# Performance work log

Hardware: AMD Instinct MI355X
Metric: run time of the kernel (lower is better)

The kernel has to match this reference:

```python
import jax, jax.numpy as jnp
import numpy as np

B, C, N, T = 64, 16, 4096, 12   # batch, channels, num_nodes, timesteps
APT = 10                        # adaptive-embedding size
NUM_SUPPORTS = 3                # 2 fixed + 1 adaptive
ORDER = 2                       # diffusion hops


def _rand_adj(k):
    # random row-stochastic transition matrix (stand-in for normalized graph support)
    a = jax.random.uniform(k, (N, N), jnp.float32)
    return a / jnp.sum(a, axis=1, keepdims=True)


def setup_inputs() -> dict:
    key = jax.random.key(0)
    ks = jax.random.split(key, 7)
    x = jax.random.normal(ks[0], (B, C, N, T), jnp.float32)
    support0 = _rand_adj(ks[1])
    support1 = _rand_adj(ks[2])
    nodevec1 = jax.random.normal(ks[3], (N, APT), jnp.float32)
    nodevec2 = jax.random.normal(ks[4], (APT, N), jnp.float32)
    c_cat = C * (NUM_SUPPORTS * ORDER + 1)  # 7*C
    W = jax.random.normal(ks[5], (C, c_cat), jnp.float32) * 0.05  # 1x1 conv weight
    b = jnp.zeros((C,), jnp.float32)
    return dict(x=x, support0=support0, support1=support1,
                nodevec1=nodevec1, nodevec2=nodevec2, W=W, b=b)


def _nconv(x, a):
    # torch: einsum('ncvl,vw->ncwl')
    return jnp.einsum('bcnt,nm->bcmt', x, a)


def reference(x, support0, support1, nodevec1, nodevec2, W, b):
    # adaptive adjacency: softmax(relu(E1 @ E2), dim=1)
    adp = jax.nn.softmax(jax.nn.relu(nodevec1 @ nodevec2), axis=1)
    supports = [support0, support1, adp]
    outs = [x]
    for a in supports:  # small fixed loop over supports/hops
        x1 = _nconv(x, a)
        outs.append(x1)
        x2 = _nconv(x1, a)
        outs.append(x2)
    h = jnp.concatenate(outs, axis=1)            # [B, 7C, N, T]
    h = jnp.einsum('bknt,ck->bcnt', h, W) + b[None, :, None, None]  # 1x1 conv
    # dropout omitted (eval mode / deterministic reference)
    return x + h                                  # residual add
```

## Files before the change

kernel.cpp:

```cpp
#include <hip/hip_runtime.h>
#include <hip/hip_bf16.h>

#define B_  64
#define C_  16
#define N_  4096
#define T_  12
#define ROWS_ (B_ * T_ * C_)
#define NT_ 64

typedef __attribute__((ext_vector_type(4))) float f32x4;
typedef __attribute__((ext_vector_type(8))) short s16x8;
typedef __attribute__((ext_vector_type(4))) short s16x4;
typedef __attribute__((ext_vector_type(8))) int   i32x8;
typedef __attribute__((ext_vector_type(4))) int   i32x4;

__device__ __forceinline__ ushort f2bf(float f) {
    unsigned u = __builtin_bit_cast(unsigned, f);
    u += 0x7fffu + ((u >> 16) & 1u);
    return (ushort)(u >> 16);
}

__device__ __forceinline__ uchar f2fp8(float f) {
    float a = fabsf(f);
    unsigned s = (__builtin_bit_cast(unsigned, f) >> 24) & 0x80u;
    if (a >= 448.f) return (uchar)(s | 0x7E);
    if (a < 0.015625f) {
        int m = (int)rintf(a * 512.f);
        return (uchar)(s | (unsigned)m);
    }
    unsigned u = __builtin_bit_cast(unsigned, a);
    unsigned r = (u + 0x7FFFFu + ((u >> 20) & 1u)) >> 20;
    return (uchar)(s | (r - 960u));
}

__device__ __forceinline__ f32x4 mfma16x16x16bf16(s16x4 a, s16x4 b, f32x4 c) {
#if __has_builtin(__builtin_amdgcn_mfma_f32_16x16x16_bf16)
    return __builtin_amdgcn_mfma_f32_16x16x16_bf16(a, b, c, 0, 0, 0);
#elif __has_builtin(__builtin_amdgcn_mfma_f32_16x16x16bf16_1k)
    return __builtin_amdgcn_mfma_f32_16x16x16bf16_1k(a, b, c, 0, 0, 0);
#else
    f32x4 d = c;
    asm volatile("v_mfma_f32_16x16x16_bf16 %0, %1, %2, %0"
                 : "+v"(d) : "v"(a), "v"(b));
    return d;
#endif
}

typedef const __attribute__((address_space(1))) unsigned int* gas_t;
typedef __attribute__((address_space(3))) unsigned int* las_t;
__device__ __forceinline__ void gload16(const ushort* g, ushort* l) {
    __builtin_amdgcn_global_load_lds((gas_t)(const void*)g, (las_t)(void*)l, 16, 0, 0);
}
__device__ __forceinline__ void gload16b(const uchar* g, uchar* l) {
    __builtin_amdgcn_global_load_lds((gas_t)(const void*)g, (las_t)(void*)l, 16, 0, 0);
}

__global__ __launch_bounds__(256)
void pack_x(const float* __restrict__ x, ushort* __restrict__ X2,
            uchar* __restrict__ X8) {
    __shared__ float xs[16][32][13];
    const int t  = threadIdx.x;
    const int n0 = blockIdx.x * 32;
    const int b  = blockIdx.y;
    #pragma unroll
    for (int p0 = 0; p0 < 2; ++p0) {
        int p = p0 * 256 + t;
        int c = p >> 5, nn = p & 31;
        const float* src = x + (size_t)((b * 16 + c) * 4096 + n0 + nn) * 12;
        float tmp[12];
        *(float4*)(tmp)     = *(const float4*)(src);
        *(float4*)(tmp + 4) = *(const float4*)(src + 4);
        *(float4*)(tmp + 8) = *(const float4*)(src + 8);
        #pragma unroll
        for (int k = 0; k < 12; ++k) xs[c][nn][k] = tmp[k];
    }
    __syncthreads();
    #pragma unroll
    for (int i = 0; i < 24; ++i) {
        int e = i * 256 + t;
        int nn = e & 31, rowi = e >> 5;
        int tt = rowi >> 4, c = rowi & 15;
        float xv = xs[c][nn][tt];
        size_t row = (size_t)(b * 12 + tt) * 16 + c;
        X2[row * 4096 + n0 + nn] = f2bf(xv);
        X8[row * 4096 + n0 + nn] = f2fp8(xv);
    }
}

__global__ __launch_bounds__(256)
void transpose_fp8(const float* __restrict__ S, uchar* __restrict__ D, float scale) {
    __shared__ float ld[64][65];
    const int t  = threadIdx.x;
    const int m0 = blockIdx.x * 64;
    const int n0 = blockIdx.y * 64;
    #pragma unroll
    for (int it = 0; it < 4; ++it) {
        int row = it * 16 + (t >> 4);
        int col = (t & 15) * 4;
        float4 v = *(const float4*)&S[(size_t)(n0 + row) * 4096 + m0 + col];
        ld[row][col] = v.x; ld[row][col + 1] = v.y;
        ld[row][col + 2] = v.z; ld[row][col + 3] = v.w;
    }
    __syncthreads();
    #pragma unroll
    for (int it = 0; it < 8; ++it) {
        int mr = it * 8 + (t >> 5);
        int nc = (t & 31) * 2;
        ushort p = (ushort)f2fp8(ld[nc][mr] * scale) |
                   ((ushort)f2fp8(ld[nc + 1][mr] * scale) << 8);
        *(ushort*)&D[(size_t)(m0 + mr) * 4096 + n0 + nc] = p;
    }
}

__global__ __launch_bounds__(256)
void adp_rows(const float* __restrict__ e1, const float* __restrict__ e2,
              float* __restrict__ maxn, float* __restrict__ sumn) {
    const int n = blockIdx.x, t = threadIdx.x;
    __shared__ float se1[10];
    __shared__ float red[8];
    if (t < 10) se1[t] = e1[n * 10 + t];
    __syncthreads();
    float v[16];
    float mx = -1e30f;
    #pragma unroll
    for (int i = 0; i < 16; ++i) {
        int m = i * 256 + t;
        float s = 0.f;
        #pragma unroll
        for (int k = 0; k < 10; ++k) s += se1[k] * e2[k * 4096 + m];
        s = fmaxf(s, 0.f);
        v[i] = s;
        mx = fmaxf(mx, s);
    }
    for (int o = 32; o; o >>= 1) mx = fmaxf(mx, __shfl_down(mx, o));
    if ((t & 63) == 0) red[t >> 6] = mx;
    __syncthreads();
    if (t == 0) red[4] = fmaxf(fmaxf(red[0], red[1]), fmaxf(red[2], red[3]));
    __syncthreads();
    mx = red[4];
    float sm = 0.f;
    #pragma unroll
    for (int i = 0; i < 16; ++i) sm += __expf(v[i] - mx);
    for (int o = 32; o; o >>= 1) sm += __shfl_down(sm, o);
    __syncthreads();
    if ((t & 63) == 0) red[t >> 6] = sm;
    __syncthreads();
    if (t == 0) { maxn[n] = mx; sumn[n] = red[0] + red[1] + red[2] + red[3]; }
}

__global__ __launch_bounds__(256)
void adp_make(const float* __restrict__ e1, const float* __restrict__ e2,
              const float* __restrict__ maxn, const float* __restrict__ sumn,
              ushort* __restrict__ D) {
    __shared__ float se1[64][10];
    __shared__ float se2[10][64];
    const int t  = threadIdx.x;
    const int m0 = blockIdx.x * 64;
    const int n0 = blockIdx.y * 64;
    for (int i = t; i < 640; i += 256) ((float*)se1)[i] = e1[n0 * 10 + i];
    for (int i = t; i < 640; i += 256) {
        int k = i >> 6, m = i & 63;
        se2[k][m] = e2[k * 4096 + m0 + m];
    }
    __syncthreads();
    #pragma unroll
    for (int it = 0; it < 8; ++it) {
        int mr = it * 8 + (t >> 5);
        int nc = (t & 31) * 2;
        float v0 = 0.f, v1 = 0.f;
        #pragma unroll
        for (int k = 0; k < 10; ++k) {
            float e2v = se2[k][mr];
            v0 += se1[nc][k] * e2v;
            v1 += se1[nc + 1][k] * e2v;
        }
        v0 = fmaxf(v0, 0.f);
        v1 = fmaxf(v1, 0.f);
        float va = __expf(v0 - maxn[n0 + nc])     / sumn[n0 + nc];
        float vb = __expf(v1 - maxn[n0 + nc + 1]) / sumn[n0 + nc + 1];
        unsigned pack = (unsigned)f2bf(va) | ((unsigned)f2bf(vb) << 16);
        *(unsigned*)&D[(size_t)(m0 + mr) * 4096 + n0 + nc] = pack;
    }
}

__global__ __launch_bounds__(512, 2)
void gemm_mix(const ushort* __restrict__ Xp, const ushort* __restrict__ Bt,
              ushort* __restrict__ Yp, float* __restrict__ racc,
              const float* __restrict__ W, int cblk, int writeY, int initR) {
    __shared__ ushort lds[65536];
    const int tid  = threadIdx.x;
    const int lane = tid & 63;
    const int wid  = tid >> 6;
    const int wm   = wid >> 2;
    const int wn   = wid & 3;
    const int lr   = lane & 15;
    const int lq   = lane >> 4;
    const int fsw  = (lane & 7) << 3;

    int flat = blockIdx.y * gridDim.x + blockIdx.x;
    int swz  = (flat & 7) * 96 + (flat >> 3);
    const size_t r0 = (size_t)(swz >> 4) * 256;
    const size_t c0 = (size_t)(swz & 15) * 256;

#define AIDX(b, mi, ks) (((b) * 32768)          + (((((mi) * 32 + wm * 16 + lr) * 64) + (ks) * 32 + lq * 8) ^ fsw))
#define BIDX(b, nj, ks) (((b) * 32768 + 16384)  + ((((wn * 64 + (nj) * 16 + lr) * 64) + (ks) * 32 + lq * 8) ^ fsw))

#define STAGE(P, rg0, tt, h, mat)                                                      \
    {                                                                                  \
        ushort* _base = &lds[((tt) & 1) * 32768 + (mat) * 16384 + (h) * 8192];         \
        const size_t _k0 = (size_t)(tt) * 64;                                          \
        _Pragma("unroll")                                                              \
        for (int _i = 0; _i < 2; ++_i) {                                               \
            int _e   = (_i * 512 + tid) * 8;                                           \
            int _row = _e >> 6;                                                        \
            int _col = (_e & 63) ^ ((_row & 7) << 3);                                  \
            gload16(&(P)[((rg0) + (h) * 128 + _row) * 4096 + _k0 + _col], &_base[_e]); \
        }                                                                              \
    }

#define PHASE(MI0, STAGE_STMT)                                                                                 \
    {                                                                                                          \
        STAGE_STMT;                                                                                            \
        s16x8 a0 = *(const s16x8*)&lds[AIDX(b, (MI0),     0)];                                                 \
        s16x8 a1 = *(const s16x8*)&lds[AIDX(b, (MI0),     1)];                                                 \
        s16x8 a2 = *(const s16x8*)&lds[AIDX(b, (MI0) + 1, 0)];                                                 \
        s16x8 a3 = *(const s16x8*)&lds[AIDX(b, (MI0) + 1, 1)];                                                 \
        __builtin_amdgcn_s_barrier();                                                                          \
        __builtin_amdgcn_s_setprio(1);                                                                         \
        _Pragma("unroll")                                                                                      \
        for (int nj = 0; nj < 4; ++nj) {                                                                       \
            acc[(MI0)][nj]     = __builtin_amdgcn_mfma_f32_16x16x32_bf16(a0, bfr[nj][0], acc[(MI0)][nj], 0, 0, 0);     \
            acc[(MI0)][nj]     = __builtin_amdgcn_mfma_f32_16x16x32_bf16(a1, bfr[nj][1], acc[(MI0)][nj], 0, 0, 0);     \
            acc[(MI0) + 1][nj] = __builtin_amdgcn_mfma_f32_16x16x32_bf16(a2, bfr[nj][0], acc[(MI0) + 1][nj], 0, 0, 0); \
            acc[(MI0) + 1][nj] = __builtin_amdgcn_mfma_f32_16x16x32_bf16(a3, bfr[nj][1], acc[(MI0) + 1][nj], 0, 0, 0); \
        }                                                                                                      \
        __builtin_amdgcn_s_setprio(0);                                                                         \
    }

    f32x4 acc[8][4] = {};

    STAGE(Xp, r0, 0, 0, 0);
    STAGE(Xp, r0, 0, 1, 0);
    STAGE(Bt, c0, 0, 0, 1);
    STAGE(Bt, c0, 0, 1, 1);
    STAGE(Xp, r0, 1, 0, 0);
    STAGE(Bt, c0, 1, 0, 1);
    asm volatile("s_waitcnt vmcnt(4)" ::: "memory");
    __builtin_amdgcn_s_barrier();

    for (int t = 0; t < NT_; ++t) {
        const int b = t & 1;
        s16x8 bfr[4][2];
        if (t + 1 < NT_) STAGE(Xp, r0, t + 1, 1, 0);
        #pragma unroll
        for (int nj = 0; nj < 4; ++nj) {
            bfr[nj][0] = *(const s16x8*)&lds[BIDX(b, nj, 0)];
            bfr[nj][1] = *(const s16x8*)&lds[BIDX(b, nj, 1)];
        }
        PHASE(0, {});
        __builtin_amdgcn_s_barrier();
        PHASE(2, { if (t + 1 < NT_) STAGE(Bt, c0, t + 1, 1, 1); });
        __builtin_amdgcn_s_barrier();
        PHASE(4, { if (t + 2 < NT_) STAGE(Xp, r0, t + 2, 0, 0); });
        __builtin_amdgcn_s_barrier();
        PHASE(6, { if (t + 2 < NT_) STAGE(Bt, c0, t + 2, 0, 1); });
        if (t < NT_ - 2)       { asm volatile("s_waitcnt vmcnt(4)" ::: "memory"); }
        else if (t == NT_ - 2) { asm volatile("s_waitcnt vmcnt(0)" ::: "memory"); }
        __builtin_amdgcn_sched_barrier(0);
        __builtin_amdgcn_s_barrier();
    }

    if (writeY) {
        #pragma unroll
        for (int mi = 0; mi < 8; ++mi) {
            #pragma unroll
            for (int nj = 0; nj < 4; ++nj) {
                const int col = wn * 64 + nj * 16 + lr;
                #pragma unroll
                for (int r = 0; r < 4; ++r) {
                    const int rr = mi * 32 + wm * 16 + lq * 4 + r;
                    lds[(rr * 256 + col) ^ ((rr & 7) << 3)] = f2bf(acc[mi][nj][r]);
                }
            }
        }
        __syncthreads();
        #pragma unroll
        for (int it = 0; it < 16; ++it) {
            int e = it * 4096 + tid * 8;
            int row = e >> 8, colu = e & 255;
            s16x8 v = *(const s16x8*)&lds[e ^ ((row & 7) << 3)];
            *(s16x8*)&Yp[(r0 + row) * 4096 + c0 + colu] = v;
        }
    }

    {
        const float4 wv4 = *(const float4*)&W[(size_t)lr * 112 + cblk + lq * 4];
        s16x4 wf;
        wf[0] = (short)f2bf(wv4.x); wf[1] = (short)f2bf(wv4.y);
        wf[2] = (short)f2bf(wv4.z); wf[3] = (short)f2bf(wv4.w);
        #pragma unroll
        for (int mi = 0; mi < 8; ++mi) {
            #pragma unroll
            for (int nj = 0; nj < 4; ++nj) {
                s16x4 cb;
                cb[0] = (short)f2bf(acc[mi][nj][0]); cb[1] = (short)f2bf(acc[mi][nj][1]);
                cb[2] = (short)f2bf(acc[mi][nj][2]); cb[3] = (short)f2bf(acc[mi][nj][3]);
                f32x4 d = mfma16x16x16bf16(wf, cb, (f32x4){0.f, 0.f, 0.f, 0.f});
                const size_t row = r0 + (size_t)mi * 32 + wm * 16 + lq * 4;
                const size_t col = c0 + wn * 64 + nj * 16 + lr;
                if (initR) {
                    #pragma unroll
                    for (int r = 0; r < 4; ++r) racc[(row + r) * 4096 + col] = d[r];
                } else {
                    #pragma unroll
                    for (int r = 0; r < 4; ++r) {
                        float* p = &racc[(row + r) * 4096 + col];
                        *p += d[r];
                    }
                }
            }
        }
    }
#undef AIDX
#undef BIDX
#undef STAGE
#undef PHASE
}

__device__ __forceinline__ i32x8 ldfrag8(const uchar* lds8, int rbase, int row, int lq) {
    const int sw = (row & 7) << 4;
    const int b  = rbase + row * 128;
    i32x4 lo = *(const i32x4*)&lds8[b + ((lq * 32) ^ sw)];
    i32x4 hi = *(const i32x4*)&lds8[b + ((lq * 32 + 16) ^ sw)];
    return (i32x8){lo[0], lo[1], lo[2], lo[3], hi[0], hi[1], hi[2], hi[3]};
}

__global__ __launch_bounds__(512, 2)
void gemm_fp8(const uchar* __restrict__ Xp, const uchar* __restrict__ Bt,
              uchar* __restrict__ Yp, float* __restrict__ racc,
              const float* __restrict__ W, int cblk, int writeY, int initR,
              int sA, int sB, float ysc) {
    __shared__ uchar lds8[131072];
    const int tid  = threadIdx.x;
    const int lane = tid & 63;
    const int wid  = tid >> 6;
    const int wm   = wid >> 2;
    const int wn   = wid & 3;
    const int lr   = lane & 15;
    const int lq   = lane >> 4;

    int flat = blockIdx.y * gridDim.x + blockIdx.x;
    int swz  = (flat & 7) * 96 + (flat >> 3);
    const size_t r0 = (size_t)(swz >> 4) * 256;
    const size_t c0 = (size_t)(swz & 15) * 256;

#define STAGE8(P, rg0, tt, h, mat)                                                       \
    {                                                                                    \
        uchar* _base = &lds8[((tt) & 1) * 65536 + (mat) * 32768 + (h) * 16384];          \
        const size_t _k0 = (size_t)(tt) * 128;                                           \
        _Pragma("unroll")                                                                \
        for (int _i = 0; _i < 2; ++_i) {                                                 \
            int _e   = (_i * 512 + tid) * 16;                                            \
            int _row = _e >> 7;                                                          \
            int _col = (_e & 127) ^ ((_row & 7) << 4);                                   \
            gload16b(&(P)[((rg0) + (h) * 128 + _row) * 4096 + _k0 + _col], &_base[_e]);  \
        }                                                                                \
    }

    f32x4 acc[8][4] = {};

    STAGE8(Xp, r0, 0, 0, 0);
    STAGE8(Xp, r0, 0, 1, 0);
    STAGE8(Bt, c0, 0, 0, 1);
    STAGE8(Bt, c0, 0, 1, 1);
    STAGE8(Xp, r0, 1, 0, 0);
    STAGE8(Bt, c0, 1, 0, 1);
    asm volatile("s_waitcnt vmcnt(4)" ::: "memory");
    __builtin_amdgcn_s_barrier();

    for (int t = 0; t < 32; ++t) {
        const int bb = (t & 1) * 65536;
        i32x8 bf[4];
        if (t + 1 < 32) STAGE8(Xp, r0, t + 1, 1, 0);
        #pragma unroll
        for (int nj = 0; nj < 4; ++nj)
            bf[nj] = ldfrag8(lds8, bb + 32768, wn * 64 + nj * 16 + lr, lq);
        i32x8 af0 = ldfrag8(lds8, bb,       wm * 16 + lr, lq);
        i32x8 af1 = ldfrag8(lds8, bb,  32 + wm * 16 + lr, lq);
        i32x8 af2 = ldfrag8(lds8, bb,  64 + wm * 16 + lr, lq);
        i32x8 af3 = ldfrag8(lds8, bb,  96 + wm * 16 + lr, lq);
        if (t + 1 < 32) STAGE8(Bt, c0, t + 1, 1, 1);
        __builtin_amdgcn_s_barrier();
        __builtin_amdgcn_s_setprio(1);
        #pragma unroll
        for (int nj = 0; nj < 4; ++nj) {
            acc[0][nj] = __builtin_amdgcn_mfma_scale_f32_16x16x128_f8f6f4(af0, bf[nj], acc[0][nj], 0, 0, 0, sA, 0, sB);
            acc[1][nj] = __builtin_amdgcn_mfma_scale_f32_16x16x128_f8f6f4(af1, bf[nj], acc[1][nj], 0, 0, 0, sA, 0, sB);
            acc[2][nj] = __builtin_amdgcn_mfma_scale_f32_16x16x128_f8f6f4(af2, bf[nj], acc[2][nj], 0, 0, 0, sA, 0, sB);
            acc[3][nj] = __builtin_amdgcn_mfma_scale_f32_16x16x128_f8f6f4(af3, bf[nj], acc[3][nj], 0, 0, 0, sA, 0, sB);
        }
        __builtin_amdgcn_s_setprio(0);
        __builtin_amdgcn_s_barrier();
        if (t + 2 < 32) STAGE8(Xp, r0, t + 2, 0, 0);
        af0 = ldfrag8(lds8, bb, 128 + wm * 16 + lr, lq);
        af1 = ldfrag8(lds8, bb, 160 + wm * 16 + lr, lq);
        af2 = ldfrag8(lds8, bb, 192 + wm * 16 + lr, lq);
        af3 = ldfrag8(lds8, bb, 224 + wm * 16 + lr, lq);
        if (t + 2 < 32) STAGE8(Bt, c0, t + 2, 0, 1);
        __builtin_amdgcn_s_barrier();
        __builtin_amdgcn_s_setprio(1);
        #pragma unroll
        for (int nj = 0; nj < 4; ++nj) {
            acc[4][nj] = __builtin_amdgcn_mfma_scale_f32_16x16x128_f8f6f4(af0, bf[nj], acc[4][nj], 0, 0, 0, sA, 0, sB);
            acc[5][nj] = __builtin_amdgcn_mfma_scale_f32_16x16x128_f8f6f4(af1, bf[nj], acc[5][nj], 0, 0, 0, sA, 0, sB);
            acc[6][nj] = __builtin_amdgcn_mfma_scale_f32_16x16x128_f8f6f4(af2, bf[nj], acc[6][nj], 0, 0, 0, sA, 0, sB);
            acc[7][nj] = __builtin_amdgcn_mfma_scale_f32_16x16x128_f8f6f4(af3, bf[nj], acc[7][nj], 0, 0, 0, sA, 0, sB);
        }
        __builtin_amdgcn_s_setprio(0);
        if (t < 30)       { asm volatile("s_waitcnt vmcnt(4)" ::: "memory"); }
        else if (t == 30) { asm volatile("s_waitcnt vmcnt(0)" ::: "memory"); }
        __builtin_amdgcn_sched_barrier(0);
        __builtin_amdgcn_s_barrier();
    }

    if (writeY) {
        #pragma unroll
        for (int mi = 0; mi < 8; ++mi) {
            #pragma unroll
            for (int nj = 0; nj < 4; ++nj) {
                const int col = wn * 64 + nj * 16 + lr;
                #pragma unroll
                for (int r = 0; r < 4; ++r) {
                    const int rr = mi * 32 + wm * 16 + lq * 4 + r;
                    lds8[(rr * 256 + col) ^ ((rr & 7) << 4)] = f2fp8(acc[mi][nj][r] * ysc);
                }
            }
        }
        __syncthreads();
        #pragma unroll
        for (int it = 0; it < 8; ++it) {
            int e = it * 8192 + tid * 16;
            int row = e >> 8, colu = e & 255;
            i32x4 v = *(const i32x4*)&lds8[e ^ ((row & 7) << 4)];
            *(i32x4*)&Yp[(r0 + row) * 4096 + c0 + colu] = v;
        }
    }

    {
        const float4 wv4 = *(const float4*)&W[(size_t)lr * 112 + cblk + lq * 4];
        s16x4 wf;
        wf[0] = (short)f2bf(wv4.x); wf[1] = (short)f2bf(wv4.y);
        wf[2] = (short)f2bf(wv4.z); wf[3] = (short)f2bf(wv4.w);
        #pragma unroll
        for (int mi = 0; mi < 8; ++mi) {
            #pragma unroll
            for (int nj = 0; nj < 4; ++nj) {
                s16x4 cb;
                cb[0] = (short)f2bf(acc[mi][nj][0]); cb[1] = (short)f2bf(acc[mi][nj][1]);
                cb[2] = (short)f2bf(acc[mi][nj][2]); cb[3] = (short)f2bf(acc[mi][nj][3]);
                f32x4 d = mfma16x16x16bf16(wf, cb, (f32x4){0.f, 0.f, 0.f, 0.f});
                const size_t row = r0 + (size_t)mi * 32 + wm * 16 + lq * 4;
                const size_t col = c0 + wn * 64 + nj * 16 + lr;
                if (initR) {
                    #pragma unroll
                    for (int r = 0; r < 4; ++r) racc[(row + r) * 4096 + col] = d[r];
                } else {
                    #pragma unroll
                    for (int r = 0; r < 4; ++r) {
                        float* p = &racc[(row + r) * 4096 + col];
                        *p += d[r];
                    }
                }
            }
        }
    }
#undef STAGE8
}

__global__ __launch_bounds__(256)
void final_out(const float* __restrict__ racc, const float* __restrict__ x,
               const float* __restrict__ W, const float* __restrict__ bias,
               float* __restrict__ out) {
    __shared__ float fr[192][32];
    __shared__ float xs[16][32][13];
    __shared__ float sW[16][16];
    __shared__ float sb[16];
    const int t  = threadIdx.x;
    const int n0 = blockIdx.x * 32;
    const int b  = blockIdx.y;
    sW[t >> 4][t & 15] = W[(t >> 4) * 112 + (t & 15)];
    if (t < 16) sb[t] = bias[t];
    #pragma unroll
    for (int i = 0; i < 24; ++i) {
        int e = i * 256 + t;
        int rr = e >> 5, nn = e & 31;
        fr[rr][nn] = racc[((size_t)b * 192 + rr) * 4096 + n0 + nn];
    }
    #pragma unroll
    for (int p0 = 0; p0 < 2; ++p0) {
        int p = p0 * 256 + t;
        int c = p >> 5, nn = p & 31;
        const float* src = x + (size_t)((b * 16 + c) * 4096 + n0 + nn) * 12;
        float tmp[12];
        *(float4*)(tmp)     = *(const float4*)(src);
        *(float4*)(tmp + 4) = *(const float4*)(src + 4);
        *(float4*)(tmp + 8) = *(const float4*)(src + 8);
        #pragma unroll
        for (int k = 0; k < 12; ++k) xs[c][nn][k] = tmp[k];
    }
    __syncthreads();
    #pragma unroll
    for (int p0 = 0; p0 < 2; ++p0) {
        int p = p0 * 256 + t;
        int c = p >> 5, nn = p & 31;
        float buf[12];
        #pragma unroll
        for (int tt = 0; tt < 12; ++tt) {
            float acc = xs[c][nn][tt] + sb[c] + fr[tt * 16 + c][nn];
            #pragma unroll
            for (int cp = 0; cp < 16; ++cp) acc += sW[c][cp] * xs[cp][nn][tt];
            buf[tt] = acc;
        }
        float* dst = &out[(size_t)((b * 16 + c) * 4096 + n0 + nn) * 12];
        *(float4*)(dst)     = *(float4*)(buf);
        *(float4*)(dst + 4) = *(float4*)(buf + 4);
        *(float4*)(dst + 8) = *(float4*)(buf + 8);
    }
}

extern "C" void kernel_launch(void* const* d_in, const int* in_sizes, int n_in,
                              void* d_out, int out_size, void* d_ws, size_t ws_size,
                              hipStream_t stream) {
    const float* x    = (const float*)d_in[0];
    const float* s0   = (const float*)d_in[1];
    const float* s1   = (const float*)d_in[2];
    const float* e1   = (const float*)d_in[3];
    const float* e2   = (const float*)d_in[4];
    const float* W    = (const float*)d_in[5];
    const float* bias = (const float*)d_in[6];
    float* out = (float*)d_out;

    char* ws = (char*)d_ws;
    const size_t SZ_X2   = (size_t)ROWS_ * 4096 * 2;
    const size_t SZ_RACC = (size_t)ROWS_ * 4096 * 4;
    const size_t SZ_REGA = SZ_X2;
    const size_t SZ_X8   = (size_t)ROWS_ * 4096;
    const size_t SZ_SF   = (size_t)4096 * 4096;

    ushort* X2   = (ushort*)(ws);
    float*  racc = (float*)(ws + SZ_X2);
    char*   REGA = ws + SZ_X2 + SZ_RACC;
    uchar*  X8   = (uchar*)(REGA + SZ_REGA);
    uchar*  SF   = (uchar*)((char*)X8 + SZ_X8);
    ushort* ADT  = (ushort*)((char*)SF + SZ_SF);
    float*  maxn = (float*)((char*)ADT + (size_t)4096 * 4096 * 2);
    float*  sumn = maxn + 4096;

    uchar*  Y80   = (uchar*)REGA;
    uchar*  Y81   = (uchar*)REGA + SZ_X8;
    ushort* Y1adp = (ushort*)REGA;

    const int S_ONE = 0x7F7F7F7F;
    const int S_M6  = 0x79797979;
    const int S_M12 = 0x73737373;

    pack_x<<<dim3(128, 64), 256, 0, stream>>>(x, X2, X8);
    transpose_fp8<<<dim3(64, 64), 256, 0, stream>>>(s0, SF, 4096.f);
    adp_rows<<<4096, 256, 0, stream>>>(e1, e2, maxn, sumn);
    adp_make<<<dim3(64, 64), 256, 0, stream>>>(e1, e2, maxn, sumn, ADT);

    gemm_fp8<<<dim3(16, 48), 512, 0, stream>>>(X8,  SF, Y80, racc, W, 16, 1, 1, S_ONE, S_M12, 64.f);
    gemm_fp8<<<dim3(16, 48), 512, 0, stream>>>(Y80, SF, Y80, racc, W, 32, 0, 0, S_M6,  S_M12, 0.f);
    transpose_fp8<<<dim3(64, 64), 256, 0, stream>>>(s1, SF, 4096.f);
    gemm_fp8<<<dim3(16, 48), 512, 0, stream>>>(X8,  SF, Y81, racc, W, 48, 1, 0, S_ONE, S_M12, 64.f);
    gemm_fp8<<<dim3(16, 48), 512, 0, stream>>>(Y81, SF, Y81, racc, W, 64, 0, 0, S_M6,  S_M12, 0.f);
    gemm_mix<<<dim3(16, 48), 512, 0, stream>>>(X2,    ADT, Y1adp, racc, W, 80, 1, 0);
    gemm_mix<<<dim3(16, 48), 512, 0, stream>>>(Y1adp, ADT, Y1adp, racc, W, 96, 0, 0);

    final_out<<<dim3(128, 64), 256, 0, stream>>>(racc, x, W, bias, out);
}
```

Baseline: 2.213 ms.

## Defer channel mixing to final kernel, drop fp32 accumulator read-modify-write

GEMM epilogues no longer run an MFMA channel mix with read-modify-write into a large fp32 accumulator; each GEMM writes only its low-precision output to a separate buffer. A new final kernel decodes all six fp8/bf16 intermediates per timestep and applies the full 1x1 conv weight plus residual. This aims to remove repeated fp32 global RMW traffic. In exchange it adds more workspace buffers, fp8 decoding and a heavier final kernel with per-timestep synchronization, and hop-2 fp8 precision now affects the output directly.

```diff
diff --git a/kernel.cpp b/kernel.cpp
--- a/kernel.cpp
+++ b/kernel.cpp
@@ -10,7 +10,6 @@
 
 typedef __attribute__((ext_vector_type(4))) float f32x4;
 typedef __attribute__((ext_vector_type(8))) short s16x8;
-typedef __attribute__((ext_vector_type(4))) short s16x4;
 typedef __attribute__((ext_vector_type(8))) int   i32x8;
 typedef __attribute__((ext_vector_type(4))) int   i32x4;
 
@@ -18,6 +17,9 @@
     unsigned u = __builtin_bit_cast(unsigned, f);
     u += 0x7fffu + ((u >> 16) & 1u);
     return (ushort)(u >> 16);
+}
+__device__ __forceinline__ float bf2f(ushort v) {
+    return __builtin_bit_cast(float, (unsigned)v << 16);
 }
 
 __device__ __forceinline__ uchar f2fp8(float f) {
@@ -33,17 +35,12 @@
     return (uchar)(s | (r - 960u));
 }
 
-__device__ __forceinline__ f32x4 mfma16x16x16bf16(s16x4 a, s16x4 b, f32x4 c) {
-#if __has_builtin(__builtin_amdgcn_mfma_f32_16x16x16_bf16)
-    return __builtin_amdgcn_mfma_f32_16x16x16_bf16(a, b, c, 0, 0, 0);
-#elif __has_builtin(__builtin_amdgcn_mfma_f32_16x16x16bf16_1k)
-    return __builtin_amdgcn_mfma_f32_16x16x16bf16_1k(a, b, c, 0, 0, 0);
-#else
-    f32x4 d = c;
-    asm volatile("v_mfma_f32_16x16x16_bf16 %0, %1, %2, %0"
-                 : "+v"(d) : "v"(a), "v"(b));
-    return d;
-#endif
+__device__ __forceinline__ float fp8dec(uchar v) {
+    unsigned e = (v >> 3) & 0xFu;
+    unsigned m = v & 7u;
+    float mag = e ? __builtin_bit_cast(float, ((e + 120u) << 23) | (m << 20))
+                  : (float)m * 0.001953125f;
+    return (v & 0x80u) ? -mag : mag;
 }
 
 typedef const __attribute__((address_space(1))) unsigned int* gas_t;
@@ -184,9 +181,8 @@
 }
 
 __global__ __launch_bounds__(512, 2)
-void gemm_mix(const ushort* __restrict__ Xp, const ushort* __restrict__ Bt,
-              ushort* __restrict__ Yp, float* __restrict__ racc,
-              const float* __restrict__ W, int cblk, int writeY, int initR) {
+void gemm_bf16(const ushort* __restrict__ Xp, const ushort* __restrict__ Bt,
+               ushort* __restrict__ Yp) {
     __shared__ ushort lds[65536];
     const int tid  = threadIdx.x;
     const int lane = tid & 63;
@@ -270,56 +266,25 @@
         __builtin_amdgcn_s_barrier();
     }
 
-    if (writeY) {
-        #pragma unroll
-        for (int mi = 0; mi < 8; ++mi) {
+    #pragma unroll
+    for (int mi = 0; mi < 8; ++mi) {
+        #pragma unroll
+        for (int nj = 0; nj < 4; ++nj) {
+            const int col = wn * 64 + nj * 16 + lr;
             #pragma unroll
-            for (int nj = 0; nj < 4; ++nj) {
-                const int col = wn * 64 + nj * 16 + lr;
-                #pragma unroll
-                for (int r = 0; r < 4; ++r) {
-                    const int rr = mi * 32 + wm * 16 + lq * 4 + r;
-                    lds[(rr * 256 + col) ^ ((rr & 7) << 3)] = f2bf(acc[mi][nj][r]);
-                }
+            for (int r = 0; r < 4; ++r) {
+                const int rr = mi * 32 + wm * 16 + lq * 4 + r;
+                lds[(rr * 256 + col) ^ ((rr & 7) << 3)] = f2bf(acc[mi][nj][r]);
             }
         }
-        __syncthreads();
-        #pragma unroll
-        for (int it = 0; it < 16; ++it) {
-            int e = it * 4096 + tid * 8;
-            int row = e >> 8, colu = e & 255;
-            s16x8 v = *(const s16x8*)&lds[e ^ ((row & 7) << 3)];
-            *(s16x8*)&Yp[(r0 + row) * 4096 + c0 + colu] = v;
-        }
-    }
-
-    {
-        const float4 wv4 = *(const float4*)&W[(size_t)lr * 112 + cblk + lq * 4];
-        s16x4 wf;
-        wf[0] = (short)f2bf(wv4.x); wf[1] = (short)f2bf(wv4.y);
-        wf[2] = (short)f2bf(wv4.z); wf[3] = (short)f2bf(wv4.w);
-        #pragma unroll
-        for (int mi = 0; mi < 8; ++mi) {
-            #pragma unroll
-            for (int nj = 0; nj < 4; ++nj) {
-                s16x4 cb;
-                cb[0] = (short)f2bf(acc[mi][nj][0]); cb[1] = (short)f2bf(acc[mi][nj][1]);
-                cb[2] = (short)f2bf(acc[mi][nj][2]); cb[3] = (short)f2bf(acc[mi][nj][3]);
-                f32x4 d = mfma16x16x16bf16(wf, cb, (f32x4){0.f, 0.f, 0.f, 0.f});
-                const size_t row = r0 + (size_t)mi * 32 + wm * 16 + lq * 4;
-                const size_t col = c0 + wn * 64 + nj * 16 + lr;
-                if (initR) {
-                    #pragma unroll
-                    for (int r = 0; r < 4; ++r) racc[(row + r) * 4096 + col] = d[r];
-                } else {
-                    #pragma unroll
-                    for (int r = 0; r < 4; ++r) {
-                        float* p = &racc[(row + r) * 4096 + col];
-                        *p += d[r];
-                    }
-                }
-            }
-        }
+    }
+    __syncthreads();
+    #pragma unroll
+    for (int it = 0; it < 16; ++it) {
+        int e = it * 4096 + tid * 8;
+        int row = e >> 8, colu = e & 255;
+        s16x8 v = *(const s16x8*)&lds[e ^ ((row & 7) << 3)];
+        *(s16x8*)&Yp[(r0 + row) * 4096 + c0 + colu] = v;
     }
 #undef AIDX
 #undef BIDX
@@ -337,9 +302,7 @@
 
 __global__ __launch_bounds__(512, 2)
 void gemm_fp8(const uchar* __restrict__ Xp, const uchar* __restrict__ Bt,
-              uchar* __restrict__ Yp, float* __restrict__ racc,
-              const float* __restrict__ W, int cblk, int writeY, int initR,
-              int sA, int sB, float ysc) {
+              uchar* __restrict__ Yp, int sA, int sB, float ysc) {
     __shared__ uchar lds8[131072];
     const int tid  = threadIdx.x;
     const int lane = tid & 63;
@@ -423,79 +386,45 @@
         __builtin_amdgcn_s_barrier();
     }
 
-    if (writeY) {
-        #pragma unroll
-        for (int mi = 0; mi < 8; ++mi) {
+    #pragma unroll
+    for (int mi = 0; mi < 8; ++mi) {
+        #pragma unroll
+        for (int nj = 0; nj < 4; ++nj) {
+            const int col = wn * 64 + nj * 16 + lr;
             #pragma unroll
-            for (int nj = 0; nj < 4; ++nj) {
-                const int col = wn * 64 + nj * 16 + lr;
-                #pragma unroll
-                for (int r = 0; r < 4; ++r) {
-                    const int rr = mi * 32 + wm * 16 + lq * 4 + r;
-                    lds8[(rr * 256 + col) ^ ((rr & 7) << 4)] = f2fp8(acc[mi][nj][r] * ysc);
-                }
+            for (int r = 0; r < 4; ++r) {
+                const int rr = mi * 32 + wm * 16 + lq * 4 + r;
+                lds8[(rr * 256 + col) ^ ((rr & 7) << 4)] = f2fp8(acc[mi][nj][r] * ysc);
             }
         }
-        __syncthreads();
-        #pragma unroll
-        for (int it = 0; it < 8; ++it) {
-            int e = it * 8192 + tid * 16;
-            int row = e >> 8, colu = e & 255;
-            i32x4 v = *(const i32x4*)&lds8[e ^ ((row & 7) << 4)];
-            *(i32x4*)&Yp[(r0 + row) * 4096 + c0 + colu] = v;
-        }
-    }
-
-    {
-        const float4 wv4 = *(const float4*)&W[(size_t)lr * 112 + cblk + lq * 4];
-        s16x4 wf;
-        wf[0] = (short)f2bf(wv4.x); wf[1] = (short)f2bf(wv4.y);
-        wf[2] = (short)f2bf(wv4.z); wf[3] = (short)f2bf(wv4.w);
-        #pragma unroll
-        for (int mi = 0; mi < 8; ++mi) {
-            #pragma unroll
-            for (int nj = 0; nj < 4; ++nj) {
-                s16x4 cb;
-                cb[0] = (short)f2bf(acc[mi][nj][0]); cb[1] = (short)f2bf(acc[mi][nj][1]);
-                cb[2] = (short)f2bf(acc[mi][nj][2]); cb[3] = (short)f2bf(acc[mi][nj][3]);
-                f32x4 d = mfma16x16x16bf16(wf, cb, (f32x4){0.f, 0.f, 0.f, 0.f});
-                const size_t row = r0 + (size_t)mi * 32 + wm * 16 + lq * 4;
-                const size_t col = c0 + wn * 64 + nj * 16 + lr;
-                if (initR) {
-                    #pragma unroll
-                    for (int r = 0; r < 4; ++r) racc[(row + r) * 4096 + col] = d[r];
-                } else {
-                    #pragma unroll
-                    for (int r = 0; r < 4; ++r) {
-                        float* p = &racc[(row + r) * 4096 + col];
-                        *p += d[r];
-                    }
-                }
-            }
-        }
+    }
+    __syncthreads();
+    #pragma unroll
+    for (int it = 0; it < 8; ++it) {
+        int e = it * 8192 + tid * 16;
+        int row = e >> 8, colu = e & 255;
+        i32x4 v = *(const i32x4*)&lds8[e ^ ((row & 7) << 4)];
+        *(i32x4*)&Yp[(r0 + row) * 4096 + c0 + colu] = v;
     }
 #undef STAGE8
 }
 
 __global__ __launch_bounds__(256)
-void final_out(const float* __restrict__ racc, const float* __restrict__ x,
+void final_mix(const float* __restrict__ x,
+               const uchar* __restrict__ Y1s0, const uchar* __restrict__ Y2s0,
+               const uchar* __restrict__ Y1s1, const uchar* __restrict__ Y2s1,
+               const ushort* __restrict__ Y1a, const ushort* __restrict__ Y2a,
                const float* __restrict__ W, const float* __restrict__ bias,
                float* __restrict__ out) {
-    __shared__ float fr[192][32];
+    __shared__ float sW[16][112];
+    __shared__ float sb[16];
     __shared__ float xs[16][32][13];
-    __shared__ float sW[16][16];
-    __shared__ float sb[16];
+    __shared__ float ys[6][16][32];
     const int t  = threadIdx.x;
     const int n0 = blockIdx.x * 32;
     const int b  = blockIdx.y;
-    sW[t >> 4][t & 15] = W[(t >> 4) * 112 + (t & 15)];
+    for (int i = t; i < 1792; i += 256) ((float*)sW)[i] = W[i];
     if (t < 16) sb[t] = bias[t];
-    #pragma unroll
-    for (int i = 0; i < 24; ++i) {
-        int e = i * 256 + t;
-        int rr = e >> 5, nn = e & 31;
-        fr[rr][nn] = racc[((size_t)b * 192 + rr) * 4096 + n0 + nn];
-    }
     #pragma unroll
     for (int p0 = 0; p0 < 2; ++p0) {
         int p = p0 * 256 + t;
@@ -508,23 +437,48 @@
         #pragma unroll
         for (int k = 0; k < 12; ++k) xs[c][nn][k] = tmp[k];
     }
-    __syncthreads();
+    float buf[2][12];
+    for (int tt = 0; tt < 12; ++tt) {
+        __syncthreads();
+        {
+            const size_t rowb = ((size_t)b * 12 + tt) * 16;
+            #pragma unroll
+            for (int i0 = 0; i0 < 2; ++i0) {
+                int i = i0 * 256 + t;
+                int cp = i >> 5, m = i & 31;
+                size_t off = (rowb + cp) * 4096 + n0 + m;
+                ys[0][cp][m] = fp8dec(Y1s0[off]) * 0.015625f;
+                ys[1][cp][m] = fp8dec(Y2s0[off]) * 0.000244140625f;
+                ys[2][cp][m] = fp8dec(Y1s1[off]) * 0.015625f;
+                ys[3][cp][m] = fp8dec(Y2s1[off]) * 0.000244140625f;
+                ys[4][cp][m] = bf2f(Y1a[off]);
+                ys[5][cp][m] = bf2f(Y2a[off]);
+            }
+        }
+        __syncthreads();
+        #pragma unroll
+        for (int p0 = 0; p0 < 2; ++p0) {
+            int p = p0 * 256 + t;
+            int c = p >> 5, nn = p & 31;
+            float acc = xs[c][nn][tt] + sb[c];
+            #pragma unroll
+            for (int cp = 0; cp < 16; ++cp) acc += sW[c][cp] * xs[cp][nn][tt];
+            #pragma unroll
+            for (int j = 0; j < 6; ++j)
+                #pragma unroll
+                for (int cp = 0; cp < 16; ++cp)
+                    acc += sW[c][16 + j * 16 + cp] * ys[j][cp][nn];
+            buf[p0][tt] = acc;
+        }
+    }
     #pragma unroll
     for (int p0 = 0; p0 < 2; ++p0) {
         int p = p0 * 256 + t;
         int c = p >> 5, nn = p & 31;
-        float buf[12];
-        #pragma unroll
-        for (int tt = 0; tt < 12; ++tt) {
-            float acc = xs[c][nn][tt] + sb[c] + fr[tt * 16 + c][nn];
-            #pragma unroll
-            for (int cp = 0; cp < 16; ++cp) acc += sW[c][cp] * xs[cp][nn][tt];
-            buf[tt] = acc;
-        }
         float* dst = &out[(size_t)((b * 16 + c) * 4096 + n0 + nn) * 12];
-        *(float4*)(dst)     = *(float4*)(buf);
-        *(float4*)(dst + 4) = *(float4*)(buf + 4);
-        *(float4*)(dst + 8) = *(float4*)(buf + 8);
+        *(float4*)(dst)     = *(float4*)(buf[p0]);
+        *(float4*)(dst + 4) = *(float4*)(buf[p0] + 4);
+        *(float4*)(dst + 8) = *(float4*)(buf[p0] + 8);
     }
 }
 
@@ -541,24 +495,22 @@
     float* out = (float*)d_out;
 
     char* ws = (char*)d_ws;
-    const size_t SZ_X2   = (size_t)ROWS_ * 4096 * 2;
-    const size_t SZ_RACC = (size_t)ROWS_ * 4096 * 4;
-    const size_t SZ_REGA = SZ_X2;
-    const size_t SZ_X8   = (size_t)ROWS_ * 4096;
-    const size_t SZ_SF   = (size_t)4096 * 4096;
+    const size_t SZ_X2 = (size_t)ROWS_ * 4096 * 2;
+    const size_t SZ_X8 = (size_t)ROWS_ * 4096;
+    const size_t SZ_SF = (size_t)4096 * 4096;
 
     ushort* X2   = (ushort*)(ws);
-    float*  racc = (float*)(ws + SZ_X2);
-    char*   REGA = ws + SZ_X2 + SZ_RACC;
-    uchar*  X8   = (uchar*)(REGA + SZ_REGA);
-    uchar*  SF   = (uchar*)((char*)X8 + SZ_X8);
-    ushort* ADT  = (ushort*)((char*)SF + SZ_SF);
-    float*  maxn = (float*)((char*)ADT + (size_t)4096 * 4096 * 2);
+    ushort* Y2a  = (ushort*)(ws);
+    uchar*  X8   = (uchar*)(ws + SZ_X2);
+    uchar*  Y1s0 = X8 + SZ_X8;
+    uchar*  Y1s1 = Y1s0 + SZ_X8;
+    uchar*  Y2s0 = Y1s1 + SZ_X8;
+    uchar*  Y2s1 = Y2s0 + SZ_X8;
+    ushort* Y1a  = (ushort*)(Y2s1 + SZ_X8);
+    uchar*  SF   = (uchar*)((char*)Y1a + SZ_X2);
+    ushort* ADT  = (ushort*)(SF + SZ_SF);
+    float*  maxn = (float*)((char*)ADT + SZ_SF * 2);
     float*  sumn = maxn + 4096;
-
-    uchar*  Y80   = (uchar*)REGA;
-    uchar*  Y81   = (uchar*)REGA + SZ_X8;
-    ushort* Y1adp = (ushort*)REGA;
 
     const int S_ONE = 0x7F7F7F7F;
     const int S_M6  = 0x79797979;
@@ -569,13 +521,14 @@
     adp_rows<<<4096, 256, 0, stream>>>(e1, e2, maxn, sumn);
     adp_make<<<dim3(64, 64), 256, 0, stream>>>(e1, e2, maxn, sumn, ADT);
 
-    gemm_fp8<<<dim3(16, 48), 512, 0, stream>>>(X8,  SF, Y80, racc, W, 16, 1, 1, S_ONE, S_M12, 64.f);
-    gemm_fp8<<<dim3(16, 48), 512, 0, stream>>>(Y80, SF, Y80, racc, W, 32, 0, 0, S_M6,  S_M12, 0.f);
+    gemm_fp8<<<dim3(16, 48), 512, 0, stream>>>(X8,   SF, Y1s0, S_ONE, S_M12, 64.f);
+    gemm_fp8<<<dim3(16, 48), 512, 0, stream>>>(Y1s0, SF, Y2s0, S_M6,  S_M12, 4096.f);
     transpose_fp8<<<dim3(64, 64), 256, 0, stream>>>(s1, SF, 4096.f);
-    gemm_fp8<<<dim3(16, 48), 512, 0, stream>>>(X8,  SF, Y81, racc, W, 48, 1, 0, S_ONE, S_M12, 64.f);
-    gemm_fp8<<<dim3(16, 48), 512, 0, stream>>>(Y81, SF, Y81, racc, W, 64, 0, 0, S_M6,  S_M12, 0.f);
-    gemm_mix<<<dim3(16, 48), 512, 0, stream>>>(X2,    ADT, Y1adp, racc, W, 80, 1, 0);
-    gemm_mix<<<dim3(16, 48), 512, 0, stream>>>(Y1adp, ADT, Y1adp, racc, W, 96, 0, 0);
-
-    final_out<<<dim3(128, 64), 256, 0, stream>>>(racc, x, W, bias, out);
-}
+    gemm_fp8<<<dim3(16, 48), 512, 0, stream>>>(X8,   SF, Y1s1, S_ONE, S_M12, 64.f);
+    gemm_fp8<<<dim3(16, 48), 512, 0, stream>>>(Y1s1, SF, Y2s1, S_M6,  S_M12, 4096.f);
+    gemm_bf16<<<dim3(16, 48), 512, 0, stream>>>(X2,  ADT, Y1a);
+    gemm_bf16<<<dim3(16, 48), 512, 0, stream>>>(Y1a, ADT, Y2a);
+
+    final_mix<<<dim3(128, 64), 256, 0, stream>>>(x, Y1s0, Y2s0, Y1s1, Y2s1,
+                                                 Y1a, Y2a, W, bias, out);
+}
```

Measured after the change: 3.163 ms. 1.43x slower.
